# Kernel optimization log

Hardware: AMD Instinct MI355X
Metric: run time of the kernel (lower is better)

The kernel has to match this reference:

```python
import jax, jax.numpy as jnp
import numpy as np

# YOLOv1 loss constants (match init_kwargs)
S, B, C = 14, 2, 20
LAMBDA_COORD, LAMBDA_NOOBJ = 5.0, 0.5
BATCH = 4096


def setup_inputs() -> dict:
    key = jax.random.key(0)
    k1, k2, k3, k4, k5 = jax.random.split(key, 5)
    N = 5 * B + C
    # predictions must be positive (torch.sqrt on w,h)
    pred = jax.random.uniform(k1, (BATCH, S, S, N), jnp.float32, 1e-3, 1.0)
    # build target exactly like convert_to_yolo_format: obj cells carry the
    # same (x,y,w,h,1) in every one of the B box slots + one-hot class;
    # empty cells are all zeros (so target[...,4]==0 is the noobj mask).
    obj = (jax.random.uniform(k2, (BATCH, S, S)) < 0.3).astype(jnp.float32)
    xy = jax.random.uniform(k3, (BATCH, S, S, 2))            # cell-relative center
    wh = jax.random.uniform(k4, (BATCH, S, S, 2), minval=0.05, maxval=0.95)
    box = jnp.concatenate([xy, wh, obj[..., None]], -1) * obj[..., None]  # [Bt,S,S,5]
    boxes = jnp.tile(box, (1, 1, 1, B))                       # [Bt,S,S,5B]
    labels = jax.random.randint(k5, (BATCH, S, S), 0, C)
    cls = jax.nn.one_hot(labels, C, dtype=jnp.float32) * obj[..., None]
    target = jnp.concatenate([boxes, cls], -1)                # [Bt,S,S,5B+C]
    return {"pred": pred, "target": target}


def _to_xyxy(box):
    # torch: xyxy[:, :2] = xy/S - 0.5*wh ; xyxy[:, 2:4] = xy/S + 0.5*wh
    c = box[..., :2] / S
    h = 0.5 * box[..., 2:4]
    return jnp.concatenate([c - h, c + h], -1)


def _yolo_loss(pred, target):
    bs = pred.shape[0]
    obj = target[..., 4] > 0                                  # [Bt,S,S] coord_mask
    pb = pred[..., :5 * B].reshape(pred.shape[:-1] + (B, 5))  # [Bt,S,S,B,5]
    tb = target[..., :5 * B].reshape(target.shape[:-1] + (B, 5))
    t0 = tb[..., 0, :]                                        # torch uses bbox_target[i] (first box)

    # IoU of each of the B predicted boxes against the cell's target box
    p4 = _to_xyxy(pb)                                         # [Bt,S,S,B,4]
    t4 = _to_xyxy(t0)[..., None, :]                           # [Bt,S,S,1,4]
    lt = jnp.maximum(p4[..., :2], t4[..., :2])
    rb = jnp.minimum(p4[..., 2:], t4[..., 2:])
    whi = jnp.clip(rb - lt, 0.0)
    inter = whi[..., 0] * whi[..., 1]
    area_p = (p4[..., 2] - p4[..., 0]) * (p4[..., 3] - p4[..., 1])
    area_t = (t4[..., 2] - t4[..., 0]) * (t4[..., 3] - t4[..., 1])
    # torch stores max_iou via .item() -> detached constant target
    iou = jax.lax.stop_gradient(inter / (area_p + area_t - inter))  # [Bt,S,S,B]
    max_iou = iou.max(-1)
    idx = iou.argmax(-1)
    resp = (idx[..., None] == jnp.arange(B)) & obj[..., None]       # responsible box mask

    rf = resp.astype(pred.dtype)
    of = obj.astype(pred.dtype)
    nf = 1.0 - of

    # coord losses (responsible boxes only)
    loss_xy = jnp.sum(rf[..., None] * (pb[..., :2] - tb[..., :2]) ** 2)
    pwh = jnp.where(resp[..., None], pb[..., 2:4], 1.0)  # safe sqrt outside mask
    twh = jnp.where(resp[..., None], tb[..., 2:4], 1.0)
    loss_wh = jnp.sum(rf[..., None] * (jnp.sqrt(pwh) - jnp.sqrt(twh)) ** 2)
    # objectness: pred conf vs (detached) max IoU
    loss_obj = jnp.sum(rf * (pb[..., 4] - max_iou[..., None]) ** 2)
    # no-object: conf channels of every box slot in empty cells
    loss_noobj = jnp.sum(nf[..., None] * (pb[..., 4] - tb[..., 4]) ** 2)
    # class loss over object cells
    loss_cls = jnp.sum(of[..., None] * (pred[..., 5 * B:] - target[..., 5 * B:]) ** 2)

    loss = (LAMBDA_COORD * (loss_xy + loss_wh) + loss_obj
            + LAMBDA_NOOBJ * loss_noobj + loss_cls) / bs
    return loss


def reference(pred, target):
    return _yolo_loss(pred, target)
```

## Files before the change

kernel.cpp:

```cpp
#include <hip/hip_runtime.h>


__global__ void zero_out_kernel(float* out) { out[0] = 0.0f; }

__device__ __forceinline__ void gll16(const void* g, void* l) {
    __builtin_amdgcn_global_load_lds(
        (const __attribute__((address_space(1))) void*)(uintptr_t)g,
        (__attribute__((address_space(3))) void*)(uintptr_t)l, 16, 0, 0);
}
__device__ __forceinline__ void gll4(const void* g, void* l) {
    __builtin_amdgcn_global_load_lds(
        (const __attribute__((address_space(1))) void*)(uintptr_t)g,
        (__attribute__((address_space(3))) void*)(uintptr_t)l, 4, 0, 0);
}

__device__ __forceinline__ void stage_tile(const float* __restrict__ g,
                                           float* lds, int lane)
{
    const char* gb = (const char*)g;
    char* lb = (char*)lds;
    #pragma unroll
    for (int i = 0; i < 7; ++i)
        gll16(gb + i * 1024 + lane * 16, lb + i * 1024);
    gll4(gb + 7168 + lane * 4, lb + 7168);
    gll4(gb + 7424 + lane * 4, lb + 7424);
}

__global__ __launch_bounds__(256, 5) void yolo_loss_kernel(
    const float* __restrict__ pred, const float* __restrict__ target,
    float* __restrict__ out)
{
    __shared__ __align__(16) float sbuf[4][1920];

    const int lane = threadIdx.x & 63;
    const int wid  = threadIdx.x >> 6;
    const size_t tile0 = ((size_t)blockIdx.x * 4 + wid) * 64;
    const float* gp = pred   + tile0 * 30;
    const float* gt = target + tile0 * 30;
    float* sw = sbuf[wid];

    float pv[30], tv[30];

    stage_tile(gp, sw, lane);
    asm volatile("s_waitcnt vmcnt(0)" ::: "memory");
    {
        const float2* rp = (const float2*)&sw[lane * 30];
        #pragma unroll
        for (int j = 0; j < 15; ++j) {
            float2 a = rp[j]; pv[2*j] = a.x; pv[2*j+1] = a.y;
        }
    }
    asm volatile("s_waitcnt lgkmcnt(0)" ::: "memory");

    stage_tile(gt, sw, lane);
    asm volatile("s_waitcnt vmcnt(0)" ::: "memory");
    {
        const float2* rt = (const float2*)&sw[lane * 30];
        #pragma unroll
        for (int j = 0; j < 15; ++j) {
            float2 b = rt[j]; tv[2*j] = b.x; tv[2*j+1] = b.y;
        }
    }

    const float invS = 1.0f / 14.0f;
    const bool obj = tv[4] > 0.0f;

    float tcx = tv[0] * invS, tcy = tv[1] * invS;
    float thw = 0.5f * tv[2], thh = 0.5f * tv[3];
    float tx1 = tcx - thw, ty1 = tcy - thh;
    float tx2 = tcx + thw, ty2 = tcy + thh;
    float area_t = (tx2 - tx1) * (ty2 - ty1);

    float iou0 = 0.0f, iou1 = 0.0f;
    #pragma unroll
    for (int b = 0; b < 2; ++b) {
        float cx = pv[5*b + 0] * invS, cy = pv[5*b + 1] * invS;
        float hw = 0.5f * pv[5*b + 2], hh = 0.5f * pv[5*b + 3];
        float x1 = cx - hw, y1 = cy - hh, x2 = cx + hw, y2 = cy + hh;
        float lx = fmaxf(x1, tx1), ly = fmaxf(y1, ty1);
        float rx = fminf(x2, tx2), ry = fminf(y2, ty2);
        float w = fmaxf(rx - lx, 0.0f), h = fmaxf(ry - ly, 0.0f);
        float inter = w * h;
        float area_p = (x2 - x1) * (y2 - y1);
        float iou = inter / (area_p + area_t - inter);
        if (b == 0) iou0 = iou; else iou1 = iou;
    }
    const bool  sel     = iou1 > iou0;
    const float max_iou = fmaxf(iou0, iou1);

    float local;
    if (obj) {
        float pbx = sel ? pv[5] : pv[0];
        float pby = sel ? pv[6] : pv[1];
        float pbw = sel ? pv[7] : pv[2];
        float pbh = sel ? pv[8] : pv[3];
        float pbc = sel ? pv[9] : pv[4];

        float dx = pbx - tv[0], dy = pby - tv[1];
        float loss_xy = dx*dx + dy*dy;

        float sw_ = sqrtf(pbw) - sqrtf(tv[2]);
        float sh_ = sqrtf(pbh) - sqrtf(tv[3]);
        float loss_wh = sw_*sw_ + sh_*sh_;

        float dob = pbc - max_iou;
        float loss_obj = dob * dob;

        float loss_cls = 0.0f;
        #pragma unroll
        for (int c = 0; c < 20; ++c) {
            float d = pv[10 + c] - tv[10 + c];
            loss_cls = fmaf(d, d, loss_cls);
        }
        local = 5.0f * (loss_xy + loss_wh) + loss_obj + loss_cls;
    } else {
        float d0 = pv[4] - tv[4];
        float d1 = pv[9] - tv[9];
        local = 0.5f * (d0*d0 + d1*d1);
    }

    #pragma unroll
    for (int off = 32; off > 0; off >>= 1)
        local += __shfl_down(local, off, 64);

    __shared__ float wsum[4];
    if (lane == 0) wsum[wid] = local;
    __syncthreads();
    if (threadIdx.x == 0) {
        float s = wsum[0] + wsum[1] + wsum[2] + wsum[3];
        atomicAdd(out, s * (1.0f / 4096.0f));
    }
}

extern "C" void kernel_launch(void* const* d_in, const int* in_sizes, int n_in,
                              void* d_out, int out_size, void* d_ws, size_t ws_size,
                              hipStream_t stream) {
    const float* pred   = (const float*)d_in[0];
    const float* target = (const float*)d_in[1];
    float* out = (float*)d_out;

    zero_out_kernel<<<1, 1, 0, stream>>>(out);
    yolo_loss_kernel<<<3136, 256, 0, stream>>>(pred, target, out);
}
```

Measured before the change: 204.0 us.

## Use persistent single-wave blocks with double-buffered LDS prefetch of tiles

Replaces the one-tile-per-wave grid (3136 blocks of 256 threads) with 1280 persistent 64-thread blocks that loop over the 12544 tiles. Each iteration prefetches the next tile's pred and target into the other LDS buffer via global_load_lds and waits only on the older batch (vmcnt(18)), so loads overlap with compute. Pred and target are now staged together rather than one after the other. This cuts the number of blocks and atomics and hides memory latency. The cost is fewer waves resident per CU (occupancy set by the 30 KB LDS per block), which may reduce memory-level parallelism on a bandwidth-bound kernel.

Result: no change. 206.6 us (+1.3%).

```diff
diff --git a/kernel.cpp b/kernel.cpp
--- a/kernel.cpp
+++ b/kernel.cpp
@@ -1,5 +1,8 @@
 #include <hip/hip_runtime.h>
 
+
+#define NT   12544
+#define NBLK 1280
 
 __global__ void zero_out_kernel(float* out) { out[0] = 0.0f; }
 
@@ -14,122 +17,127 @@
         (__attribute__((address_space(3))) void*)(uintptr_t)l, 4, 0, 0);
 }
 
-__device__ __forceinline__ void stage_tile(const float* __restrict__ g,
+__device__ __forceinline__ void stage_tile(const float* __restrict__ gp,
+                                           const float* __restrict__ gt,
                                            float* lds, int lane)
 {
-    const char* gb = (const char*)g;
-    char* lb = (char*)lds;
+    const char* pb = (const char*)gp;
+    const char* tb = (const char*)gt;
+    char* lp = (char*)lds;
+    char* lt = lp + 7680;
     #pragma unroll
     for (int i = 0; i < 7; ++i)
-        gll16(gb + i * 1024 + lane * 16, lb + i * 1024);
-    gll4(gb + 7168 + lane * 4, lb + 7168);
-    gll4(gb + 7424 + lane * 4, lb + 7424);
+        gll16(pb + i * 1024 + lane * 16, lp + i * 1024);
+    gll4(pb + 7168 + lane * 4, lp + 7168);
+    gll4(pb + 7424 + lane * 4, lp + 7424);
+    #pragma unroll
+    for (int i = 0; i < 7; ++i)
+        gll16(tb + i * 1024 + lane * 16, lt + i * 1024);
+    gll4(tb + 7168 + lane * 4, lt + 7168);
+    gll4(tb + 7424 + lane * 4, lt + 7424);
 }
 
-__global__ __launch_bounds__(256, 5) void yolo_loss_kernel(
+__global__ __launch_bounds__(64) void yolo_loss_kernel(
     const float* __restrict__ pred, const float* __restrict__ target,
     float* __restrict__ out)
 {
-    __shared__ __align__(16) float sbuf[4][1920];
+    __shared__ __align__(16) float sbuf[2][3840];
 
-    const int lane = threadIdx.x & 63;
-    const int wid  = threadIdx.x >> 6;
-    const size_t tile0 = ((size_t)blockIdx.x * 4 + wid) * 64;
-    const float* gp = pred   + tile0 * 30;
-    const float* gt = target + tile0 * 30;
-    float* sw = sbuf[wid];
+    const int lane = threadIdx.x;
+    const float invS = 1.0f / 14.0f;
 
-    float pv[30], tv[30];
+    float acc = 0.0f;
+    int t = blockIdx.x;
+    stage_tile(pred + (size_t)t * 1920, target + (size_t)t * 1920,
+               sbuf[0], lane);
+    int cur = 0;
 
-    stage_tile(gp, sw, lane);
-    asm volatile("s_waitcnt vmcnt(0)" ::: "memory");
-    {
-        const float2* rp = (const float2*)&sw[lane * 30];
+    while (t < NT) {
+        const int tn = t + NBLK;
+        if (tn < NT) {
+            stage_tile(pred + (size_t)tn * 1920, target + (size_t)tn * 1920,
+                       sbuf[cur ^ 1], lane);
+            asm volatile("s_waitcnt vmcnt(18)" ::: "memory");
+        } else {
+            asm volatile("s_waitcnt vmcnt(0)" ::: "memory");
+        }
+
+        float pv[30], tv[30];
+        const float2* rp = (const float2*)&sbuf[cur][lane * 30];
+        const float2* rt = (const float2*)&sbuf[cur][1920 + lane * 30];
         #pragma unroll
         for (int j = 0; j < 15; ++j) {
             float2 a = rp[j]; pv[2*j] = a.x; pv[2*j+1] = a.y;
-        }
-    }
-    asm volatile("s_waitcnt lgkmcnt(0)" ::: "memory");
-
-    stage_tile(gt, sw, lane);
-    asm volatile("s_waitcnt vmcnt(0)" ::: "memory");
-    {
-        const float2* rt = (const float2*)&sw[lane * 30];
-        #pragma unroll
-        for (int j = 0; j < 15; ++j) {
             float2 b = rt[j]; tv[2*j] = b.x; tv[2*j+1] = b.y;
         }
-    }
+        asm volatile("s_waitcnt lgkmcnt(0)" ::: "memory");
 
-    const float invS = 1.0f / 14.0f;
-    const bool obj = tv[4] > 0.0f;
+        const bool obj = tv[4] > 0.0f;
 
-    float tcx = tv[0] * invS, tcy = tv[1] * invS;
-    float thw = 0.5f * tv[2], thh = 0.5f * tv[3];
-    float tx1 = tcx - thw, ty1 = tcy - thh;
-    float tx2 = tcx + thw, ty2 = tcy + thh;
-    float area_t = (tx2 - tx1) * (ty2 - ty1);
+        float tcx = tv[0] * invS, tcy = tv[1] * invS;
+        float thw = 0.5f * tv[2], thh = 0.5f * tv[3];
+        float tx1 = tcx - thw, ty1 = tcy - thh;
+        float tx2 = tcx + thw, ty2 = tcy + thh;
+        float area_t = (tx2 - tx1) * (ty2 - ty1);
 
-    float iou0 = 0.0f, iou1 = 0.0f;
-    #pragma unroll
-    for (int b = 0; b < 2; ++b) {
-        float cx = pv[5*b + 0] * invS, cy = pv[5*b + 1] * invS;
-        float hw = 0.5f * pv[5*b + 2], hh = 0.5f * pv[5*b + 3];
-        float x1 = cx - hw, y1 = cy - hh, x2 = cx + hw, y2 = cy + hh;
-        float lx = fmaxf(x1, tx1), ly = fmaxf(y1, ty1);
-        float rx = fminf(x2, tx2), ry = fminf(y2, ty2);
-        float w = fmaxf(rx - lx, 0.0f), h = fmaxf(ry - ly, 0.0f);
-        float inter = w * h;
-        float area_p = (x2 - x1) * (y2 - y1);
-        float iou = inter / (area_p + area_t - inter);
-        if (b == 0) iou0 = iou; else iou1 = iou;
-    }
-    const bool  sel     = iou1 > iou0;
-    const float max_iou = fmaxf(iou0, iou1);
+        float iou0 = 0.0f, iou1 = 0.0f;
+        #pragma unroll
+        for (int b = 0; b < 2; ++b) {
+            float cx = pv[5*b + 0] * invS, cy = pv[5*b + 1] * invS;
+            float hw = 0.5f * pv[5*b + 2], hh = 0.5f * pv[5*b + 3];
+            float x1 = cx - hw, y1 = cy - hh, x2 = cx + hw, y2 = cy + hh;
+            float lx = fmaxf(x1, tx1), ly = fmaxf(y1, ty1);
+            float rx = fminf(x2, tx2), ry = fminf(y2, ty2);
+            float w = fmaxf(rx - lx, 0.0f), h = fmaxf(ry - ly, 0.0f);
+            float inter = w * h;
+            float area_p = (x2 - x1) * (y2 - y1);
+            float iou = inter / (area_p + area_t - inter);
+            if (b == 0) iou0 = iou; else iou1 = iou;
+        }
+        const bool  sel     = iou1 > iou0;
+        const float max_iou = fmaxf(iou0, iou1);
 
-    float local;
-    if (obj) {
-        float pbx = sel ? pv[5] : pv[0];
-        float pby = sel ? pv[6] : pv[1];
-        float pbw = sel ? pv[7] : pv[2];
-        float pbh = sel ? pv[8] : pv[3];
-        float pbc = sel ? pv[9] : pv[4];
+        float local;
+        if (obj) {
+            float pbx = sel ? pv[5] : pv[0];
+            float pby = sel ? pv[6] : pv[1];
+            float pbw = sel ? pv[7] : pv[2];
+            float pbh = sel ? pv[8] : pv[3];
+            float pbc = sel ? pv[9] : pv[4];
 
-        float dx = pbx - tv[0], dy = pby - tv[1];
-        float loss_xy = dx*dx + dy*dy;
+            float dx = pbx - tv[0], dy = pby - tv[1];
+            float loss_xy = dx*dx + dy*dy;
 
-        float sw_ = sqrtf(pbw) - sqrtf(tv[2]);
-        float sh_ = sqrtf(pbh) - sqrtf(tv[3]);
-        float loss_wh = sw_*sw_ + sh_*sh_;
+            float sw_ = sqrtf(pbw) - sqrtf(tv[2]);
+            float sh_ = sqrtf(pbh) - sqrtf(tv[3]);
+            float loss_wh = sw_*sw_ + sh_*sh_;
 
-        float dob = pbc - max_iou;
-        float loss_obj = dob * dob;
+            float dob = pbc - max_iou;
+            float loss_obj = dob * dob;
 
-        float loss_cls = 0.0f;
-        #pragma unroll
-        for (int c = 0; c < 20; ++c) {
-            float d = pv[10 + c] - tv[10 + c];
-            loss_cls = fmaf(d, d, loss_cls);
+            float loss_cls = 0.0f;
+            #pragma unroll
+            for (int c = 0; c < 20; ++c) {
+                float d = pv[10 + c] - tv[10 + c];
+                loss_cls = fmaf(d, d, loss_cls);
+            }
+            local = 5.0f * (loss_xy + loss_wh) + loss_obj + loss_cls;
+        } else {
+            float d0 = pv[4] - tv[4];
+            float d1 = pv[9] - tv[9];
+            local = 0.5f * (d0*d0 + d1*d1);
         }
-        local = 5.0f * (loss_xy + loss_wh) + loss_obj + loss_cls;
-    } else {
-        float d0 = pv[4] - tv[4];
-        float d1 = pv[9] - tv[9];
-        local = 0.5f * (d0*d0 + d1*d1);
+        acc += local;
+
+        cur ^= 1;
+        t = tn;
     }
 
     #pragma unroll
     for (int off = 32; off > 0; off >>= 1)
-        local += __shfl_down(local, off, 64);
-
-    __shared__ float wsum[4];
-    if (lane == 0) wsum[wid] = local;
-    __syncthreads();
-    if (threadIdx.x == 0) {
-        float s = wsum[0] + wsum[1] + wsum[2] + wsum[3];
-        atomicAdd(out, s * (1.0f / 4096.0f));
-    }
+        acc += __shfl_down(acc, off, 64);
+    if (lane == 0)
+        atomicAdd(out, acc * (1.0f / 4096.0f));
 }
 
 extern "C" void kernel_launch(void* const* d_in, const int* in_sizes, int n_in,
@@ -140,5 +148,5 @@
     float* out = (float*)d_out;
 
     zero_out_kernel<<<1, 1, 0, stream>>>(out);
-    yolo_loss_kernel<<<3136, 256, 0, stream>>>(pred, target, out);
+    yolo_loss_kernel<<<NBLK, 64, 0, stream>>>(pred, target, out);
 }
```
